# Performance work log

Hardware: AMD Instinct MI355X
Metric: run time of the kernel (lower is better)

The kernel has to match this reference:

```python
import jax, jax.numpy as jnp
import numpy as np

N, E, K, D = 100000, 3200000, 1024, 11


def setup_inputs() -> dict:
    key = jax.random.key(0)
    ks = jax.random.split(key, 11)
    return {
        "x": jax.random.normal(ks[0], (N, D), jnp.float32),
        "edge_index": jax.random.randint(ks[1], (2, E), 0, N, dtype=jnp.int32),
        "ready_idx": jnp.sort(jax.random.randint(ks[2], (K,), 0, N, dtype=jnp.int32)),
        "W1": jax.random.normal(ks[3], (D, 64), jnp.float32) * 0.2,
        "b1": jax.random.normal(ks[4], (64,), jnp.float32) * 0.02,
        "W2": jax.random.normal(ks[5], (75, 1), jnp.float32) * 0.2,
        "b2": jax.random.normal(ks[6], (1,), jnp.float32) * 0.02,
        "Wd": jax.random.normal(ks[7], (64, 1), jnp.float32) * 0.2,
        "bd": jax.random.normal(ks[8], (1,), jnp.float32) * 0.02,
        "Wv": jax.random.normal(ks[9], (64, 1), jnp.float32) * 0.2,
        "bv": jax.random.normal(ks[10], (1,), jnp.float32) * 0.02,
    }


def gcn_conv(x, W, b, src, dst):
    """PyG GCNConv with flow='target_to_source': gather from dst, aggregate at src.
    Symmetric normalization with self-loops (weight 1)."""
    n = x.shape[0]
    h = x @ W  # [N, F_out]
    loop = jnp.arange(n, dtype=src.dtype)
    s = jnp.concatenate([src, loop])  # aggregation index (row for target_to_source)
    d = jnp.concatenate([dst, loop])  # gather index
    deg = jax.ops.segment_sum(jnp.ones(s.shape, h.dtype), s, num_segments=n)
    dis = jnp.where(deg > 0, jax.lax.rsqrt(jnp.maximum(deg, 1e-12)), 0.0)
    norm = dis[s] * dis[d]  # [E+N]
    out = jax.ops.segment_sum(norm[:, None] * h[d], s, num_segments=n)
    return out + b


def reference(x, edge_index, ready_idx, W1, b1, W2, b2, Wd, bd, Wv, bv):
    src, dst = edge_index[0], edge_index[1]
    h = jax.nn.relu(gcn_conv(x, W1, b1, src, dst))           # [N, 64]
    x_input = jnp.concatenate([h, x], axis=1)                # [N, 75]
    probs_n = gcn_conv(x_input, W2, b2, src, dst)            # [N, 1]
    x_mean = jnp.mean(h, axis=0)                             # [64]
    v = x_mean @ Wv + bv                                     # [1]
    prob_nothing = x_mean @ Wd + bd                          # [1]
    logits = jnp.concatenate([probs_n[ready_idx, 0], prob_nothing])  # [K+1]
    probs = jax.nn.softmax(logits)
    return probs, v
```

## Files before the change

### kernel.cpp

```cpp
#include <hip/hip_runtime.h>
#include <hip/hip_fp16.h>
#include <math.h>

#define N_ 100000
#define E_ 3200000
#define K_ 1024
#define D_ 11
#define NBUCK_ 391
#define NPAD_ (NBUCK_ * 256)
#define CAPB_ 16384
#define CAP_ 32
#define CAPW_ 33
#define GB_ 512
#define CHUNK_ 6256
#define SA_ 8
#define SD_ 8
#define SP_ 4
#define XC_ 32

static inline size_t align512(size_t x) { return (x + 511) & ~(size_t)511; }

__device__ inline float2 h2f(unsigned int u) {
    __half2 h = *reinterpret_cast<__half2*>(&u);
    return __half22float2(h);
}

__global__ void k_prep(const float* __restrict__ x, const int* __restrict__ ready,
                       __half* __restrict__ xh,
                       int* __restrict__ deg, float* __restrict__ pr_raw,
                       unsigned char* __restrict__ flag, float* __restrict__ xpart,
                       int* __restrict__ bcur) {
    int i = blockIdx.x * blockDim.x + threadIdx.x;
    if (i < N_ * 16) {
        int n = i >> 4, j = i & 15;
        if (j < D_) xh[i] = __float2half_rn(x[n * D_ + j]);
    }
    if (i < N_) {
        deg[i] = 0; pr_raw[i] = 0.f;
        int lo = 0, hi = K_ - 1, f = 0;
        while (lo <= hi) {
            int mid = (lo + hi) >> 1;
            int v = ready[mid];
            if (v == i) { f = 1; break; }
            if (v < i) lo = mid + 1; else hi = mid - 1;
        }
        flag[i] = (unsigned char)f;
    }
    if (i < XC_ * 64) xpart[i] = 0.f;
    if (i < NBUCK_) bcur[i] = i * CAPB_;
}

__global__ __launch_bounds__(256) void k_bin(const int* __restrict__ src,
                                             const int* __restrict__ dst,
                                             int* __restrict__ bcur,
                                             int* __restrict__ gbuf) {
    __shared__ int sbuf[NBUCK_ * CAPW_];
    __shared__ int scnt[NBUCK_];
    int t = threadIdx.x;
    for (int b = t; b < NBUCK_; b += 256) scnt[b] = 0;
    __syncthreads();
    long e0 = (long)blockIdx.x * CHUNK_;
    for (int r = 0; r < CHUNK_; r += 2048) {
        int off = r + t * 8;
        long i0 = e0 + off;
        if (off < CHUNK_ && i0 + 7 < E_) {
            int4 s0 = *(const int4*)(src + i0);
            int4 s1 = *(const int4*)(src + i0 + 4);
            int4 d0 = *(const int4*)(dst + i0);
            int4 d1 = *(const int4*)(dst + i0 + 4);
            int ss[8] = {s0.x, s0.y, s0.z, s0.w, s1.x, s1.y, s1.z, s1.w};
            int dd[8] = {d0.x, d0.y, d0.z, d0.w, d1.x, d1.y, d1.z, d1.w};
#pragma unroll
            for (int q = 0; q < 8; q++) {
                int b = ss[q] >> 8;
                int pack = ((ss[q] & 255) << 17) | dd[q];
                int pos = atomicAdd(&scnt[b], 1);
                if (pos < CAP_) sbuf[b * CAPW_ + pos] = pack;
                else gbuf[atomicAdd(&bcur[b], 1)] = pack;
            }
        }
        __syncthreads();
        for (int b = t; b < NBUCK_; b += 256) {
            int c = min(scnt[b], CAP_);
            while (c >= 16) {
                int g = atomicAdd(&bcur[b], 16);
                c -= 16;
                if ((g & 3) == 0) {
                    int4* gp = (int4*)(gbuf + g);
#pragma unroll
                    for (int q = 0; q < 4; q++)
                        gp[q] = make_int4(sbuf[b*CAPW_ + c + 4*q],
                                          sbuf[b*CAPW_ + c + 4*q + 1],
                                          sbuf[b*CAPW_ + c + 4*q + 2],
                                          sbuf[b*CAPW_ + c + 4*q + 3]);
                } else {
                    for (int k = 0; k < 16; k++) gbuf[g + k] = sbuf[b*CAPW_ + c + k];
                }
            }
            scnt[b] = c;
        }
        __syncthreads();
    }
    for (int b = t; b < NBUCK_; b += 256) {
        int c = min(scnt[b], CAP_);
        if (c > 0) {
            int g = atomicAdd(&bcur[b], c);
            for (int k = 0; k < c; k++) gbuf[g + k] = sbuf[b*CAPW_ + k];
        }
    }
}

__global__ __launch_bounds__(256) void k_deg(const int* __restrict__ bcur,
                                             const int* __restrict__ gbuf,
                                             int* __restrict__ deg) {
    __shared__ int hist[256];
    int t = threadIdx.x, b = blockIdx.x, s = blockIdx.y;
    hist[t] = 0;
    __syncthreads();
    int base = b * CAPB_;
    int cnt = min(bcur[b] - base, CAPB_);
    int seg = (((cnt + SD_ - 1) / SD_) + 3) & ~3;
    int lo = s * seg, hi = min(lo + seg, cnt);
    int p = lo + t * 4;
    for (; p + 3 < hi; p += 1024) {
        int4 v = *(const int4*)(gbuf + base + p);
        atomicAdd(&hist[v.x >> 17], 1);
        atomicAdd(&hist[v.y >> 17], 1);
        atomicAdd(&hist[v.z >> 17], 1);
        atomicAdd(&hist[v.w >> 17], 1);
    }
    if (p < hi) {
        for (int q = p; q < hi; q++) atomicAdd(&hist[gbuf[base + q] >> 17], 1);
    }
    __syncthreads();
    int node = (b << 8) + t;
    if (node < N_ && hist[t]) atomicAdd(&deg[node], hist[t]);
}

__global__ void k_dis(const int* __restrict__ deg, float* __restrict__ dis,
                      __half* __restrict__ xh) {
    int i = blockIdx.x * blockDim.x + threadIdx.x;
    if (i >= N_) return;
    float dv = rsqrtf((float)(deg[i] + 1));
    dis[i] = dv;
    xh[(size_t)i * 16 + 11] = __float2half_rn(dv);
}

__global__ __launch_bounds__(256) void k_agg(const int* __restrict__ bcur,
                                             const int* __restrict__ gbuf,
                                             const __half* __restrict__ xh,
                                             float* __restrict__ upart) {
    __shared__ int sorted[2048];
    __shared__ int hist[256];
    __shared__ int incl[256];
    __shared__ int offa[256];
    int t = threadIdx.x, b = blockIdx.x, s = blockIdx.y;
    hist[t] = 0;
    __syncthreads();
    int base = b * CAPB_;
    int cnt = min(bcur[b] - base, CAPB_);
    int seg = (cnt + SA_ - 1) / SA_;
    int lo = s * seg, hi = min(lo + seg, cnt);
    int segn = hi - lo;
    int kmax = (segn + 255) >> 8;
    int pk[8], rk[8];
    for (int k = 0; k < kmax; k++) {
        int idx = lo + (k << 8) + t;
        if (idx < hi) {
            pk[k] = gbuf[base + idx];
            rk[k] = atomicAdd(&hist[pk[k] >> 17], 1);
        } else pk[k] = -1;
    }
    __syncthreads();
    incl[t] = hist[t];
    __syncthreads();
    for (int off = 1; off < 256; off <<= 1) {
        int v = (t >= off) ? incl[t - off] : 0;
        __syncthreads();
        incl[t] += v;
        __syncthreads();
    }
    offa[t] = incl[t] - hist[t];
    __syncthreads();
    for (int k = 0; k < kmax; k++) {
        if (pk[k] >= 0) sorted[offa[pk[k] >> 17] + rk[k]] = pk[k];
    }
    __syncthreads();
    int my_start = offa[t], my_cnt = hist[t];
    const uint4* xr = (const uint4*)xh;
    float acc[D_];
#pragma unroll
    for (int j = 0; j < D_; j++) acc[j] = 0.f;
    int i = 0;
    for (; i + 3 < my_cnt; i += 4) {
        int pp[4];
#pragma unroll
        for (int q = 0; q < 4; q++) pp[q] = sorted[my_start + i + q];
        uint4 A[4], B[4];
#pragma unroll
        for (int q = 0; q < 4; q++) {
            size_t r = (size_t)(pp[q] & 131071) * 2;
            A[q] = xr[r]; B[q] = xr[r + 1];
        }
#pragma unroll
        for (int q = 0; q < 4; q++) {
            float2 f0 = h2f(A[q].x), f1 = h2f(A[q].y), f2 = h2f(A[q].z);
            float2 f3 = h2f(A[q].w), f4 = h2f(B[q].x), f5 = h2f(B[q].y);
            float w = f5.y;
            acc[0]  = fmaf(w, f0.x, acc[0]);
            acc[1]  = fmaf(w, f0.y, acc[1]);
            acc[2]  = fmaf(w, f1.x, acc[2]);
            acc[3]  = fmaf(w, f1.y, acc[3]);
            acc[4]  = fmaf(w, f2.x, acc[4]);
            acc[5]  = fmaf(w, f2.y, acc[5]);
            acc[6]  = fmaf(w, f3.x, acc[6]);
            acc[7]  = fmaf(w, f3.y, acc[7]);
            acc[8]  = fmaf(w, f4.x, acc[8]);
            acc[9]  = fmaf(w, f4.y, acc[9]);
            acc[10] = fmaf(w, f5.x, acc[10]);
        }
    }
    for (; i < my_cnt; i++) {
        int pack = sorted[my_start + i];
        size_t r = (size_t)(pack & 131071) * 2;
        uint4 A = xr[r], B = xr[r + 1];
        float2 f0 = h2f(A.x), f1 = h2f(A.y), f2 = h2f(A.z);
        float2 f3 = h2f(A.w), f4 = h2f(B.x), f5 = h2f(B.y);
        float w = f5.y;
        acc[0]  = fmaf(w, f0.x, acc[0]);
        acc[1]  = fmaf(w, f0.y, acc[1]);
        acc[2]  = fmaf(w, f1.x, acc[2]);
        acc[3]  = fmaf(w, f1.y, acc[3]);
        acc[4]  = fmaf(w, f2.x, acc[4]);
        acc[5]  = fmaf(w, f2.y, acc[5]);
        acc[6]  = fmaf(w, f3.x, acc[6]);
        acc[7]  = fmaf(w, f3.y, acc[7]);
        acc[8]  = fmaf(w, f4.x, acc[8]);
        acc[9]  = fmaf(w, f4.y, acc[9]);
        acc[10] = fmaf(w, f5.x, acc[10]);
    }
    float* dst = upart + ((size_t)s * NPAD_ + (b << 8) + t) * 12;
    ((float4*)dst)[0] = make_float4(acc[0], acc[1], acc[2],  acc[3]);
    ((float4*)dst)[1] = make_float4(acc[4], acc[5], acc[6],  acc[7]);
    ((float4*)dst)[2] = make_float4(acc[8], acc[9], acc[10], 0.f);
}

__global__ __launch_bounds__(256) void k_red(const float* __restrict__ upart,
                                             float* __restrict__ u12) {
    int slot = blockIdx.x * blockDim.x + threadIdx.x;
    const int TOT = NPAD_ * 3;
    if (slot >= TOT) return;
    const float4* up = (const float4*)upart;
    float4 a = up[slot];
#pragma unroll
    for (int s = 1; s < SA_; s++) {
        float4 v = up[(size_t)s * TOT + slot];
        a.x += v.x; a.y += v.y; a.z += v.z; a.w += v.w;
    }
    ((float4*)u12)[slot] = a;
}

__global__ __launch_bounds__(256) void k_node(
    const float* __restrict__ u12, const float* __restrict__ x,
    const float* __restrict__ dis,
    const float* __restrict__ W1, const float* __restrict__ b1,
    const float* __restrict__ W2,
    float* __restrict__ hd, float* __restrict__ xpart) {
    __shared__ float sW1[D_ * 64];
    __shared__ float sb1[64];
    __shared__ float sW2[75];
    __shared__ float smean[64];
    int t = threadIdx.x;
    for (int k = t; k < D_ * 64; k += 256) sW1[k] = W1[k];
    if (t < 64) { sb1[t] = b1[t]; smean[t] = 0.f; }
    if (t < 75) sW2[t] = W2[t];
    __syncthreads();

    int nl = t >> 2, q = t & 3;
    int node = blockIdx.x * 64 + nl;
    bool valid = node < N_;
    float hreg[16];
    float h2v = 0.f;
    float di = 0.f;
    if (valid) {
        const float4* up = (const float4*)(u12 + (size_t)node * 12);
        float4 u0 = up[0], u1 = up[1], u2 = up[2];
        float acc[D_] = {u0.x, u0.y, u0.z, u0.w, u1.x, u1.y, u1.z, u1.w,
                         u2.x, u2.y, u2.z};
        di = dis[node];
        float xr_[D_], g[D_];
#pragma unroll
        for (int j = 0; j < D_; j++) xr_[j] = x[(size_t)node * D_ + j];
#pragma unroll
        for (int j = 0; j < D_; j++) g[j] = di * (acc[j] + di * xr_[j]);

        int fbase = q << 4;
#pragma unroll
        for (int j = 0; j < 16; j++) {
            int f = fbase + j;
            float a = sb1[f];
#pragma unroll
            for (int jj = 0; jj < D_; jj++) a = fmaf(g[jj], sW1[jj * 64 + f], a);
            float hf = fmaxf(a, 0.f);
            hreg[j] = hf;
            h2v = fmaf(hf, sW2[f], h2v);
        }
        if (q == 0) {
#pragma unroll
            for (int jj = 0; jj < D_; jj++) h2v = fmaf(xr_[jj], sW2[64 + jj], h2v);
        }
    } else {
#pragma unroll
        for (int j = 0; j < 16; j++) hreg[j] = 0.f;
    }
    h2v += __shfl_xor(h2v, 1);
    h2v += __shfl_xor(h2v, 2);
    if (valid && q == 0) hd[node] = di * h2v;

    int lane = t & 63;
#pragma unroll
    for (int j = 0; j < 16; j++) {
        float v = hreg[j];
        v += __shfl_xor(v, 4);
        v += __shfl_xor(v, 8);
        v += __shfl_xor(v, 16);
        v += __shfl_xor(v, 32);
        if (lane < 4) atomicAdd(&smean[(lane << 4) + j], v);
    }
    __syncthreads();
    if (t < 64) atomicAdd(&xpart[((blockIdx.x & (XC_ - 1)) << 6) + t], smean[t]);
}

__global__ __launch_bounds__(256) void k_pr(const int* __restrict__ bcur,
                                            const int* __restrict__ gbuf,
                                            const unsigned char* __restrict__ flag,
                                            const float* __restrict__ hd,
                                            float* __restrict__ pr_raw) {
    __shared__ float prl[256];
    __shared__ unsigned char fl[256];
    int t = threadIdx.x, b = blockIdx.x, s = blockIdx.y;
    prl[t] = 0.f;
    int node = (b << 8) + t;
    fl[t] = (node < N_) ? flag[node] : 0;
    __syncthreads();
    int base = b * CAPB_;
    int cnt = min(bcur[b] - base, CAPB_);
    int seg = (((cnt + SP_ - 1) / SP_) + 3) & ~3;
    int lo = s * seg, hi = min(lo + seg, cnt);
    int p = lo + t * 4;
    for (; p + 3 < hi; p += 1024) {
        int4 v = *(const int4*)(gbuf + base + p);
        int s0 = v.x >> 17, s1 = v.y >> 17, s2 = v.z >> 17, s3 = v.w >> 17;
        if (fl[s0]) atomicAdd(&prl[s0], hd[v.x & 131071]);
        if (fl[s1]) atomicAdd(&prl[s1], hd[v.y & 131071]);
        if (fl[s2]) atomicAdd(&prl[s2], hd[v.z & 131071]);
        if (fl[s3]) atomicAdd(&prl[s3], hd[v.w & 131071]);
    }
    if (p < hi) {
        for (int q = p; q < hi; q++) {
            int pack = gbuf[base + q];
            int sl = pack >> 17;
            if (fl[sl]) atomicAdd(&prl[sl], hd[pack & 131071]);
        }
    }
    __syncthreads();
    if (node < N_ && fl[t] && prl[t] != 0.f) atomicAdd(&pr_raw[node], prl[t]);
}

__global__ __launch_bounds__(1024) void k_final(
    const int* __restrict__ ready, const float* __restrict__ dis,
    const float* __restrict__ hd, const float* __restrict__ pr_raw,
    const float* __restrict__ xpart,
    const float* __restrict__ b2,
    const float* __restrict__ Wd, const float* __restrict__ bd,
    const float* __restrict__ Wv, const float* __restrict__ bv,
    float* __restrict__ out) {
    __shared__ float xm[64];
    __shared__ float red[1024];
    __shared__ float s_max, s_sum, s_pn, s_v;
    int t = threadIdx.x;
    if (t < 64) {
        float s = 0.f;
#pragma unroll
        for (int c = 0; c < XC_; c++) s += xpart[(c << 6) + t];
        xm[t] = s * (1.0f / N_);
    }
    __syncthreads();
    if (t == 0) {
        float pn = bd[0], vv = bv[0];
        for (int f = 0; f < 64; f++) { pn += xm[f] * Wd[f]; vv += xm[f] * Wv[f]; }
        s_pn = pn; s_v = vv;
    }
    int r = ready[t];
    float dr = dis[r];
    float l = dr * (pr_raw[r] + hd[r]) + b2[0];
    __syncthreads();
    float pn = s_pn;
    red[t] = (t == 0) ? fmaxf(l, pn) : l;
    __syncthreads();
    for (int sft = 512; sft > 0; sft >>= 1) {
        if (t < sft) red[t] = fmaxf(red[t], red[t + sft]);
        __syncthreads();
    }
    if (t == 0) s_max = red[0];
    __syncthreads();
    float m = s_max;
    float el = expf(l - m);
    red[t] = el + ((t == 0) ? expf(pn - m) : 0.f);
    __syncthreads();
    for (int sft = 512; sft > 0; sft >>= 1) {
        if (t < sft) red[t] += red[t + sft];
        __syncthreads();
    }
    if (t == 0) s_sum = red[0];
    __syncthreads();
    float inv = 1.0f / s_sum;
    out[t] = el * inv;
    if (t == 0) {
        out[K_] = expf(pn - m) * inv;
        out[K_ + 1] = s_v;
    }
}

extern "C" void kernel_launch(void* const* d_in, const int* in_sizes, int n_in,
                              void* d_out, int out_size, void* d_ws, size_t ws_size,
                              hipStream_t stream) {
    const float* x    = (const float*)d_in[0];
    const int*   ei   = (const int*)d_in[1];
    const int*   src  = ei;
    const int*   dst  = ei + E_;
    const int*   ready= (const int*)d_in[2];
    const float* W1   = (const float*)d_in[3];
    const float* b1   = (const float*)d_in[4];
    const float* W2   = (const float*)d_in[5];
    const float* b2   = (const float*)d_in[6];
    const float* Wd   = (const float*)d_in[7];
    const float* bd   = (const float*)d_in[8];
    const float* Wv   = (const float*)d_in[9];
    const float* bv   = (const float*)d_in[10];
    float* out = (float*)d_out;

    char* ws = (char*)d_ws;
    size_t o = 0;
    int*   bcur   = (int*)(ws + o);          o += align512(NBUCK_ * sizeof(int));
    int*   gbuf   = (int*)(ws + o);          o += align512((size_t)NBUCK_ * CAPB_ * sizeof(int));
    float* upart  = (float*)(ws + o);        o += align512((size_t)SA_ * NPAD_ * 12 * sizeof(float));
    float* u12    = (float*)(ws + o);        o += align512((size_t)NPAD_ * 12 * sizeof(float));
    __half* xh    = (__half*)(ws + o);       o += align512((size_t)N_ * 16 * sizeof(__half));
    int*   deg    = (int*)(ws + o);          o += align512(N_ * sizeof(int));
    float* dis    = (float*)(ws + o);        o += align512(N_ * sizeof(float));
    float* hd     = (float*)(ws + o);        o += align512(N_ * sizeof(float));
    float* pr_raw = (float*)(ws + o);        o += align512(N_ * sizeof(float));
    unsigned char* flag = (unsigned char*)(ws + o); o += align512(N_);
    float* xpart  = (float*)(ws + o);        o += align512(XC_ * 64 * sizeof(float));

    const int B = 256;
    int g_node  = (N_ + B - 1) / B;
    int g_node4 = (N_ + 63) / 64;
    int g_prep  = (N_ * 16 + B - 1) / B;
    int g_red   = (NPAD_ * 3 + B - 1) / B;
    dim3 gdeg(NBUCK_, SD_);
    dim3 gagg(NBUCK_, SA_);
    dim3 gpr(NBUCK_, SP_);

    k_prep <<<g_prep, B, 0, stream>>>(x, ready, xh, deg, pr_raw, flag, xpart, bcur);
    k_bin  <<<GB_, B, 0, stream>>>(src, dst, bcur, gbuf);
    k_deg  <<<gdeg, B, 0, stream>>>(bcur, gbuf, deg);
    k_dis  <<<g_node, B, 0, stream>>>(deg, dis, xh);
    k_agg  <<<gagg, B, 0, stream>>>(bcur, gbuf, xh, upart);
    k_red  <<<g_red, B, 0, stream>>>(upart, u12);
    k_node <<<g_node4, B, 0, stream>>>(u12, x, dis, W1, b1, W2, hd, xpart);
    k_pr   <<<gpr, B, 0, stream>>>(bcur, gbuf, flag, hd, pr_raw);
    k_final<<<1, 1024, 0, stream>>>(ready, dis, hd, pr_raw, xpart,
                                    b2, Wd, bd, Wv, bv, out);
}
```

Measured before the change: 207.9 us.

## Record ready-node edges during aggregation and drop the full second edge pass

During the first aggregation pass, the kernel now writes a compact (node, neighbor) list holding only the edges of ready-flagged nodes, spread over 32 fixed-capacity segments. The second GCN pass then becomes a small scatter over that list instead of rescanning all 3.2M binned edges. The binning kernel also flushes its shared-memory staging only once at the end rather than after each round. The risks are silent truncation if a segment fills up (8192 entries each) and extra global atomics on the segment counters.

```diff
diff --git a/kernel.cpp b/kernel.cpp
--- a/kernel.cpp
+++ b/kernel.cpp
@@ -15,8 +15,8 @@
 #define CHUNK_ 6256
 #define SA_ 8
 #define SD_ 8
-#define SP_ 4
 #define XC_ 32
+#define RSEG_ 8192
 
 static inline size_t align512(size_t x) { return (x + 511) & ~(size_t)511; }
 
@@ -29,7 +29,7 @@
                        __half* __restrict__ xh,
                        int* __restrict__ deg, float* __restrict__ pr_raw,
                        unsigned char* __restrict__ flag, float* __restrict__ xpart,
-                       int* __restrict__ bcur) {
+                       int* __restrict__ bcur, int* __restrict__ rcnt) {
     int i = blockIdx.x * blockDim.x + threadIdx.x;
     if (i < N_ * 16) {
         int n = i >> 4, j = i & 15;
@@ -48,6 +48,7 @@
     }
     if (i < XC_ * 64) xpart[i] = 0.f;
     if (i < NBUCK_) bcur[i] = i * CAPB_;
+    if (i < 32) rcnt[i] = 0;
 }
 
 __global__ __launch_bounds__(256) void k_bin(const int* __restrict__ src,
@@ -79,30 +80,25 @@
                 else gbuf[atomicAdd(&bcur[b], 1)] = pack;
             }
         }
-        __syncthreads();
-        for (int b = t; b < NBUCK_; b += 256) {
-            int c = min(scnt[b], CAP_);
-            while (c >= 16) {
-                int g = atomicAdd(&bcur[b], 16);
-                c -= 16;
-                if ((g & 3) == 0) {
-                    int4* gp = (int4*)(gbuf + g);
-#pragma unroll
-                    for (int q = 0; q < 4; q++)
-                        gp[q] = make_int4(sbuf[b*CAPW_ + c + 4*q],
-                                          sbuf[b*CAPW_ + c + 4*q + 1],
-                                          sbuf[b*CAPW_ + c + 4*q + 2],
-                                          sbuf[b*CAPW_ + c + 4*q + 3]);
-                } else {
-                    for (int k = 0; k < 16; k++) gbuf[g + k] = sbuf[b*CAPW_ + c + k];
-                }
-            }
-            scnt[b] = c;
-        }
-        __syncthreads();
-    }
+    }
+    __syncthreads();
     for (int b = t; b < NBUCK_; b += 256) {
         int c = min(scnt[b], CAP_);
+        while (c >= 16) {
+            int g = atomicAdd(&bcur[b], 16);
+            c -= 16;
+            if ((g & 3) == 0) {
+                int4* gp = (int4*)(gbuf + g);
+#pragma unroll
+                for (int q = 0; q < 4; q++)
+                    gp[q] = make_int4(sbuf[b*CAPW_ + c + 4*q],
+                                      sbuf[b*CAPW_ + c + 4*q + 1],
+                                      sbuf[b*CAPW_ + c + 4*q + 2],
+                                      sbuf[b*CAPW_ + c + 4*q + 3]);
+            } else {
+                for (int k = 0; k < 16; k++) gbuf[g + k] = sbuf[b*CAPW_ + c + k];
+            }
+        }
         if (c > 0) {
             int g = atomicAdd(&bcur[b], c);
             for (int k = 0; k < c; k++) gbuf[g + k] = sbuf[b*CAPW_ + k];
@@ -149,7 +145,10 @@
 __global__ __launch_bounds__(256) void k_agg(const int* __restrict__ bcur,
                                              const int* __restrict__ gbuf,
                                              const __half* __restrict__ xh,
-                                             float* __restrict__ upart) {
+                                             const unsigned char* __restrict__ flag,
+                                             float* __restrict__ upart,
+                                             int* __restrict__ rcnt,
+                                             int2* __restrict__ redge) {
     __shared__ int sorted[2048];
     __shared__ int hist[256];
     __shared__ int incl[256];
@@ -187,6 +186,7 @@
     }
     __syncthreads();
     int my_start = offa[t], my_cnt = hist[t];
+    int node = (b << 8) + t;
     const uint4* xr = (const uint4*)xh;
     float acc[D_];
 #pragma unroll
@@ -239,10 +239,19 @@
         acc[9]  = fmaf(w, f4.y, acc[9]);
         acc[10] = fmaf(w, f5.x, acc[10]);
     }
-    float* dst = upart + ((size_t)s * NPAD_ + (b << 8) + t) * 12;
+    float* dst = upart + ((size_t)s * NPAD_ + node) * 12;
     ((float4*)dst)[0] = make_float4(acc[0], acc[1], acc[2],  acc[3]);
     ((float4*)dst)[1] = make_float4(acc[4], acc[5], acc[6],  acc[7]);
     ((float4*)dst)[2] = make_float4(acc[8], acc[9], acc[10], 0.f);
+
+    if (node < N_ && my_cnt > 0 && flag[node]) {
+        int r = (b + s) & 31;
+        int slot = atomicAdd(&rcnt[r], my_cnt);
+        int lim = min(my_cnt, RSEG_ - slot);
+        for (int i2 = 0; i2 < lim; i2++)
+            redge[(r << 13) + slot + i2] =
+                make_int2(node, sorted[my_start + i2] & 131071);
+    }
 }
 
 __global__ __launch_bounds__(256) void k_red(const float* __restrict__ upart,
@@ -331,40 +340,15 @@
     if (t < 64) atomicAdd(&xpart[((blockIdx.x & (XC_ - 1)) << 6) + t], smean[t]);
 }
 
-__global__ __launch_bounds__(256) void k_pr(const int* __restrict__ bcur,
-                                            const int* __restrict__ gbuf,
-                                            const unsigned char* __restrict__ flag,
-                                            const float* __restrict__ hd,
-                                            float* __restrict__ pr_raw) {
-    __shared__ float prl[256];
-    __shared__ unsigned char fl[256];
-    int t = threadIdx.x, b = blockIdx.x, s = blockIdx.y;
-    prl[t] = 0.f;
-    int node = (b << 8) + t;
-    fl[t] = (node < N_) ? flag[node] : 0;
-    __syncthreads();
-    int base = b * CAPB_;
-    int cnt = min(bcur[b] - base, CAPB_);
-    int seg = (((cnt + SP_ - 1) / SP_) + 3) & ~3;
-    int lo = s * seg, hi = min(lo + seg, cnt);
-    int p = lo + t * 4;
-    for (; p + 3 < hi; p += 1024) {
-        int4 v = *(const int4*)(gbuf + base + p);
-        int s0 = v.x >> 17, s1 = v.y >> 17, s2 = v.z >> 17, s3 = v.w >> 17;
-        if (fl[s0]) atomicAdd(&prl[s0], hd[v.x & 131071]);
-        if (fl[s1]) atomicAdd(&prl[s1], hd[v.y & 131071]);
-        if (fl[s2]) atomicAdd(&prl[s2], hd[v.z & 131071]);
-        if (fl[s3]) atomicAdd(&prl[s3], hd[v.w & 131071]);
-    }
-    if (p < hi) {
-        for (int q = p; q < hi; q++) {
-            int pack = gbuf[base + q];
-            int sl = pack >> 17;
-            if (fl[sl]) atomicAdd(&prl[sl], hd[pack & 131071]);
-        }
-    }
-    __syncthreads();
-    if (node < N_ && fl[t] && prl[t] != 0.f) atomicAdd(&pr_raw[node], prl[t]);
+__global__ void k_pr(const int* __restrict__ rcnt, const int2* __restrict__ redge,
+                     const float* __restrict__ hd, float* __restrict__ pr_raw) {
+    int idx = blockIdx.x * blockDim.x + threadIdx.x;
+    int r = idx >> 13;
+    int off = idx & (RSEG_ - 1);
+    if (r < 32 && off < min(rcnt[r], RSEG_)) {
+        int2 e = redge[(r << 13) + off];
+        atomicAdd(&pr_raw[e.x], hd[e.y]);
+    }
 }
 
 __global__ __launch_bounds__(1024) void k_final(
@@ -443,10 +427,12 @@
     char* ws = (char*)d_ws;
     size_t o = 0;
     int*   bcur   = (int*)(ws + o);          o += align512(NBUCK_ * sizeof(int));
+    int*   rcnt   = (int*)(ws + o);          o += align512(32 * sizeof(int));
     int*   gbuf   = (int*)(ws + o);          o += align512((size_t)NBUCK_ * CAPB_ * sizeof(int));
     float* upart  = (float*)(ws + o);        o += align512((size_t)SA_ * NPAD_ * 12 * sizeof(float));
     float* u12    = (float*)(ws + o);        o += align512((size_t)NPAD_ * 12 * sizeof(float));
     __half* xh    = (__half*)(ws + o);       o += align512((size_t)N_ * 16 * sizeof(__half));
+    int2*  redge  = (int2*)(ws + o);         o += align512((size_t)32 * RSEG_ * sizeof(int2));
     int*   deg    = (int*)(ws + o);          o += align512(N_ * sizeof(int));
     float* dis    = (float*)(ws + o);        o += align512(N_ * sizeof(float));
     float* hd     = (float*)(ws + o);        o += align512(N_ * sizeof(float));
@@ -459,18 +445,18 @@
     int g_node4 = (N_ + 63) / 64;
     int g_prep  = (N_ * 16 + B - 1) / B;
     int g_red   = (NPAD_ * 3 + B - 1) / B;
+    int g_pr    = (32 * RSEG_) / B;
     dim3 gdeg(NBUCK_, SD_);
     dim3 gagg(NBUCK_, SA_);
-    dim3 gpr(NBUCK_, SP_);
-
-    k_prep <<<g_prep, B, 0, stream>>>(x, ready, xh, deg, pr_raw, flag, xpart, bcur);
+
+    k_prep <<<g_prep, B, 0, stream>>>(x, ready, xh, deg, pr_raw, flag, xpart, bcur, rcnt);
     k_bin  <<<GB_, B, 0, stream>>>(src, dst, bcur, gbuf);
     k_deg  <<<gdeg, B, 0, stream>>>(bcur, gbuf, deg);
     k_dis  <<<g_node, B, 0, stream>>>(deg, dis, xh);
-    k_agg  <<<gagg, B, 0, stream>>>(bcur, gbuf, xh, upart);
+    k_agg  <<<gagg, B, 0, stream>>>(bcur, gbuf, xh, flag, upart, rcnt, redge);
     k_red  <<<g_red, B, 0, stream>>>(upart, u12);
     k_node <<<g_node4, B, 0, stream>>>(u12, x, dis, W1, b1, W2, hd, xpart);
-    k_pr   <<<gpr, B, 0, stream>>>(bcur, gbuf, flag, hd, pr_raw);
+    k_pr   <<<g_pr, B, 0, stream>>>(rcnt, redge, hd, pr_raw);
     k_final<<<1, 1024, 0, stream>>>(ready, dis, hd, pr_raw, xpart,
                                     b2, Wd, bd, Wv, bv, out);
 }
```

After: 223.7 us. 7.6% more time.
